# Optimization experiments

Hardware: AMD Instinct MI355X
Metric: run time of the kernel (lower is better)

## Reference

```python
import jax, jax.numpy as jnp
import numpy as np

IN_F, OUT_F, R = 4096, 4096, 16
ALPHA = 32.0
SCALING = ALPHA / R


def setup_inputs() -> dict:
    key = jax.random.key(0)
    kx, kw, ka = jax.random.split(key, 3)
    x = jax.random.normal(kx, (4, 2048, IN_F), dtype=jnp.float32)
    # xavier_normal for weight: std = sqrt(2/(fan_in+fan_out))
    std = float(np.sqrt(2.0 / (IN_F + OUT_F)))
    weight = jax.random.normal(kw, (OUT_F, IN_F), dtype=jnp.float32) * std
    bias = jnp.zeros((OUT_F,), dtype=jnp.float32)
    A = jax.random.normal(ka, (R, IN_F), dtype=jnp.float32) * 0.01
    # B initialized to zeros in the module, but use small random values so the
    # LoRA path is numerically exercised for kernel correctness testing.
    B = jax.random.normal(jax.random.fold_in(key, 7), (OUT_F, R), dtype=jnp.float32) * 0.01
    return {"x": x, "weight": weight, "bias": bias, "A": A, "B": B}


def reference(x, weight, bias, A, B):
    # out = x @ W^T + bias + scaling * ((x @ A^T) @ B^T)
    out = jnp.einsum('bsi,oi->bso', x, weight) + bias
    xa = jnp.einsum('bsi,ri->bsr', x, A)           # [b, s, r] low-rank projection
    out = out + SCALING * jnp.einsum('bsr,or->bso', xa, B)
    return out
```

## Files before the change

### kernel.cpp

```cpp
#include <hip/hip_runtime.h>
#include <hip/hip_bf16.h>
#include <cstdint>
#include <cstddef>


#define IN_F   4096
#define OUT_F  4096
#define MROWS  8192
#define RLORA  16
#define LORA_SCALE 2.0f

#define CAST_BLOCKS 32768
#define FOLD_BLOCKS 4096

#define BM   256
#define BN   256
#define BKT  32
#define NT   (IN_F / BKT)

typedef __bf16 bf16x8 __attribute__((ext_vector_type(8)));
typedef float  f32x4  __attribute__((ext_vector_type(4)));
typedef int    i32x4  __attribute__((ext_vector_type(4)));

__device__ __forceinline__ unsigned short f2bf_rne(float f) {
    union { float f; unsigned u; } v; v.f = f;
    unsigned u = v.u;
    return (unsigned short)((u + 0x7FFFu + ((u >> 16) & 1u)) >> 16);
}

__device__ __forceinline__ void gl_lds16(const unsigned short* g, unsigned short* l) {
    __builtin_amdgcn_global_load_lds(
        (const __attribute__((address_space(1))) unsigned int*)g,
        (__attribute__((address_space(3))) unsigned int*)l,
        16, 0, 0);
}


__global__ void prep_kernel(const float* __restrict__ x,
                            const float* __restrict__ W,
                            const float* __restrict__ A,
                            const float* __restrict__ B,
                            unsigned short* __restrict__ xb,
                            unsigned short* __restrict__ wb) {
    __shared__ float sB[RLORA];
    const int bid = blockIdx.x;
    if (bid < CAST_BLOCKS) {
        int i = bid * blockDim.x + threadIdx.x;
        float4 v = ((const float4*)x)[i];
        ushort4 o;
        o.x = f2bf_rne(v.x); o.y = f2bf_rne(v.y);
        o.z = f2bf_rne(v.z); o.w = f2bf_rne(v.w);
        ((ushort4*)xb)[i] = o;
    } else {
        const int o = bid - CAST_BLOCKS;
        if (threadIdx.x < RLORA) sB[threadIdx.x] = B[o * RLORA + threadIdx.x];
        __syncthreads();
        const float4* W4  = (const float4*)(W + (size_t)o * IN_F);
        ushort4*      Wp4 = (ushort4*)(wb + (size_t)o * IN_F);
        for (int i4 = threadIdx.x; i4 < IN_F / 4; i4 += blockDim.x) {
            float4 w = W4[i4];
            float ax = 0.f, ay = 0.f, az = 0.f, aw = 0.f;
            #pragma unroll
            for (int r = 0; r < RLORA; ++r) {
                float4 a = ((const float4*)(A + (size_t)r * IN_F))[i4];
                float s = sB[r];
                ax += s * a.x; ay += s * a.y; az += s * a.z; aw += s * a.w;
            }
            w.x += LORA_SCALE * ax; w.y += LORA_SCALE * ay;
            w.z += LORA_SCALE * az; w.w += LORA_SCALE * aw;
            ushort4 ov;
            ov.x = f2bf_rne(w.x); ov.y = f2bf_rne(w.y);
            ov.z = f2bf_rne(w.z); ov.w = f2bf_rne(w.w);
            Wp4[i4] = ov;
        }
    }
}


__global__ __launch_bounds__(512, 2)
void gemm_bt_bias(const unsigned short* __restrict__ Xb,
                  const unsigned short* __restrict__ Wb,
                  const float* __restrict__ bias,
                  float* __restrict__ out) {
    __shared__ __align__(16) unsigned short smem[4 * 16384];

    const int tid  = threadIdx.x;
    const int wave = tid >> 6;
    const int lane = tid & 63;
    const int quad = lane >> 4;
    const int r16  = lane & 15;
    const int wm   = wave >> 2;
    const int wn   = wave & 3;

    const int bid = blockIdx.x;
    const int xcd = bid & 7;
    const int t   = bid >> 3;
    const int n0  = (xcd * 2 + (t & 1)) * BN;
    const int m0  = (t >> 1) * BM;

    const int qA0 = wave * 128 + lane;
    const int qA1 = qA0 + 64;
    const int rA0 = qA0 >> 2, kA0 = (qA0 & 3) ^ ((rA0 >> 1) & 3);
    const int rA1 = qA1 >> 2, kA1 = (qA1 & 3) ^ ((rA1 >> 1) & 3);

    const unsigned short* gA0 = Xb + (size_t)(m0 + rA0) * IN_F + kA0 * 8;
    const unsigned short* gA1 = Xb + (size_t)(m0 + rA1) * IN_F + kA1 * 8;
    const unsigned short* gB0 = Wb + (size_t)(n0 + rA0) * IN_F + kA0 * 8;
    const unsigned short* gB1 = Wb + (size_t)(n0 + rA1) * IN_F + kA1 * 8;

    const unsigned dA0 = wave * 1024;
    const unsigned dA1 = dA0 + 512;
    const unsigned dB0 = 8192 + wave * 1024;
    const unsigned dB1 = dB0 + 512;

    const unsigned slot  = (unsigned)(quad ^ ((r16 >> 1) & 3));
    const unsigned aoff  = (unsigned)((wm * 128 + r16) * 64) + slot * 16;
    const unsigned boff  = 16384u + (unsigned)((wn * 64 + r16) * 64) + slot * 16;
    const unsigned sbase = (unsigned)(size_t)
        ((__attribute__((address_space(3))) unsigned short*)smem);

    f32x4 acc[8][4] = {};

    #pragma unroll
    for (int s = 0; s < 3; ++s) {
        unsigned short* Lb = smem + (s << 14);
        gl_lds16(gA0, Lb + dA0); gl_lds16(gA1, Lb + dA1);
        gl_lds16(gB0, Lb + dB0); gl_lds16(gB1, Lb + dB1);
        gA0 += BKT; gA1 += BKT; gB0 += BKT; gB1 += BKT;
    }
    asm volatile("s_waitcnt vmcnt(8)" ::: "memory");
    __builtin_amdgcn_s_barrier();

    for (int p = 0; p < NT; ++p) {
        if (p + 3 < NT) {
            unsigned short* Lb = smem + (((p + 3) & 3) << 14);
            gl_lds16(gA0, Lb + dA0); gl_lds16(gA1, Lb + dA1);
            gl_lds16(gB0, Lb + dB0); gl_lds16(gB1, Lb + dB1);
            gA0 += BKT; gA1 += BKT; gB0 += BKT; gB1 += BKT;
        }

        const unsigned bufb = sbase + ((unsigned)(p & 3) << 15);
        const unsigned ab = bufb + aoff;
        const unsigned bb = bufb + boff;

        i32x4 aR[8]; i32x4 bR[4];
        asm volatile("ds_read_b128 %0, %1"             : "=v"(bR[0]) : "v"(bb));
        asm volatile("ds_read_b128 %0, %1 offset:1024" : "=v"(bR[1]) : "v"(bb));
        asm volatile("ds_read_b128 %0, %1 offset:2048" : "=v"(bR[2]) : "v"(bb));
        asm volatile("ds_read_b128 %0, %1 offset:3072" : "=v"(bR[3]) : "v"(bb));
        asm volatile("ds_read_b128 %0, %1"             : "=v"(aR[0]) : "v"(ab));
        asm volatile("ds_read_b128 %0, %1 offset:1024" : "=v"(aR[1]) : "v"(ab));
        asm volatile("ds_read_b128 %0, %1 offset:2048" : "=v"(aR[2]) : "v"(ab));
        asm volatile("ds_read_b128 %0, %1 offset:3072" : "=v"(aR[3]) : "v"(ab));
        asm volatile("ds_read_b128 %0, %1 offset:4096" : "=v"(aR[4]) : "v"(ab));
        asm volatile("ds_read_b128 %0, %1 offset:5120" : "=v"(aR[5]) : "v"(ab));
        asm volatile("ds_read_b128 %0, %1 offset:6144" : "=v"(aR[6]) : "v"(ab));
        asm volatile("ds_read_b128 %0, %1 offset:7168" : "=v"(aR[7]) : "v"(ab));

        asm volatile("s_waitcnt lgkmcnt(4)" ::: "memory");
        __builtin_amdgcn_sched_barrier(0);
        __builtin_amdgcn_s_setprio(1);
        #pragma unroll
        for (int mi = 0; mi < 4; ++mi) {
            const bf16x8 a = __builtin_bit_cast(bf16x8, aR[mi]);
            #pragma unroll
            for (int nj = 0; nj < 4; ++nj)
                acc[mi][nj] = __builtin_amdgcn_mfma_f32_16x16x32_bf16(
                    a, __builtin_bit_cast(bf16x8, bR[nj]), acc[mi][nj], 0, 0, 0);
        }
        asm volatile("s_waitcnt lgkmcnt(0)" ::: "memory");
        __builtin_amdgcn_sched_barrier(0);
        #pragma unroll
        for (int mi = 4; mi < 8; ++mi) {
            const bf16x8 a = __builtin_bit_cast(bf16x8, aR[mi]);
            #pragma unroll
            for (int nj = 0; nj < 4; ++nj)
                acc[mi][nj] = __builtin_amdgcn_mfma_f32_16x16x32_bf16(
                    a, __builtin_bit_cast(bf16x8, bR[nj]), acc[mi][nj], 0, 0, 0);
        }
        __builtin_amdgcn_sched_barrier(0);
        __builtin_amdgcn_s_setprio(0);

        if (p + 3 < NT)       { asm volatile("s_waitcnt vmcnt(8)" ::: "memory"); }
        else if (p + 3 == NT) { asm volatile("s_waitcnt vmcnt(4)" ::: "memory"); }
        else                  { asm volatile("s_waitcnt vmcnt(0)" ::: "memory"); }
        __builtin_amdgcn_s_barrier();
    }

    float bv[4];
    #pragma unroll
    for (int nj = 0; nj < 4; ++nj)
        bv[nj] = bias[n0 + wn * 64 + nj * 16 + r16];

    #pragma unroll
    for (int mi = 0; mi < 8; ++mi) {
        #pragma unroll
        for (int i = 0; i < 4; ++i) {
            const int mg = m0 + wm * 128 + mi * 16 + quad * 4 + i;
            float* orow = out + (size_t)mg * OUT_F + (n0 + wn * 64 + r16);
            #pragma unroll
            for (int nj = 0; nj < 4; ++nj)
                orow[nj * 16] = acc[mi][nj][i] + bv[nj];
        }
    }
}


extern "C" void kernel_launch(void* const* d_in, const int* in_sizes, int n_in,
                              void* d_out, int out_size, void* d_ws, size_t ws_size,
                              hipStream_t stream) {
    const float* x    = (const float*)d_in[0];
    const float* W    = (const float*)d_in[1];
    const float* bias = (const float*)d_in[2];
    const float* A    = (const float*)d_in[3];
    const float* B    = (const float*)d_in[4];
    float* out = (float*)d_out;

    unsigned short* xb = (unsigned short*)d_ws;
    unsigned short* wb = xb + (size_t)MROWS * IN_F;

    prep_kernel<<<CAST_BLOCKS + FOLD_BLOCKS, 256, 0, stream>>>(x, W, A, B, xb, wb);
    gemm_bt_bias<<<(MROWS / BM) * (OUT_F / BN), 512, 0, stream>>>(xb, wb, bias, out);
}
```

Before: 531.1 us.

## Fuse fp32-to-bf16 activation cast into GEMM load pipeline

Drops the separate pass that cast x to bf16 into workspace. The GEMM now loads fp32 x tiles into registers, converts them with packed bf16 conversion instructions, and writes them to LDS, while W still streams via direct global-to-LDS loads. The pipeline is restructured to a register-staged, two-tiles-ahead schedule, which saves a full write and re-read of the bf16 activations. In exchange the GEMM reads twice as many bytes for A, uses extra VGPRs, and has less prefetch depth.

```diff
diff --git a/kernel.cpp b/kernel.cpp
--- a/kernel.cpp
+++ b/kernel.cpp
@@ -10,9 +10,6 @@
 #define RLORA  16
 #define LORA_SCALE 2.0f
 
-#define CAST_BLOCKS 32768
-#define FOLD_BLOCKS 4096
-
 #define BM   256
 #define BN   256
 #define BKT  32
@@ -35,50 +32,87 @@
         16, 0, 0);
 }
 
-
-__global__ void prep_kernel(const float* __restrict__ x,
-                            const float* __restrict__ W,
-                            const float* __restrict__ A,
-                            const float* __restrict__ B,
-                            unsigned short* __restrict__ xb,
-                            unsigned short* __restrict__ wb) {
+__device__ __forceinline__ int cvtpk(float lo, float hi) {
+    int r;
+    asm volatile("v_cvt_pk_bf16_f32 %0, %1, %2" : "=v"(r) : "v"(lo), "v"(hi));
+    return r;
+}
+
+
+__global__ void fold_w(const float* __restrict__ W,
+                       const float* __restrict__ A,
+                       const float* __restrict__ B,
+                       unsigned short* __restrict__ wb) {
     __shared__ float sB[RLORA];
-    const int bid = blockIdx.x;
-    if (bid < CAST_BLOCKS) {
-        int i = bid * blockDim.x + threadIdx.x;
-        float4 v = ((const float4*)x)[i];
-        ushort4 o;
-        o.x = f2bf_rne(v.x); o.y = f2bf_rne(v.y);
-        o.z = f2bf_rne(v.z); o.w = f2bf_rne(v.w);
-        ((ushort4*)xb)[i] = o;
-    } else {
-        const int o = bid - CAST_BLOCKS;
-        if (threadIdx.x < RLORA) sB[threadIdx.x] = B[o * RLORA + threadIdx.x];
-        __syncthreads();
-        const float4* W4  = (const float4*)(W + (size_t)o * IN_F);
-        ushort4*      Wp4 = (ushort4*)(wb + (size_t)o * IN_F);
-        for (int i4 = threadIdx.x; i4 < IN_F / 4; i4 += blockDim.x) {
-            float4 w = W4[i4];
-            float ax = 0.f, ay = 0.f, az = 0.f, aw = 0.f;
-            #pragma unroll
-            for (int r = 0; r < RLORA; ++r) {
-                float4 a = ((const float4*)(A + (size_t)r * IN_F))[i4];
-                float s = sB[r];
-                ax += s * a.x; ay += s * a.y; az += s * a.z; aw += s * a.w;
-            }
-            w.x += LORA_SCALE * ax; w.y += LORA_SCALE * ay;
-            w.z += LORA_SCALE * az; w.w += LORA_SCALE * aw;
-            ushort4 ov;
-            ov.x = f2bf_rne(w.x); ov.y = f2bf_rne(w.y);
-            ov.z = f2bf_rne(w.z); ov.w = f2bf_rne(w.w);
-            Wp4[i4] = ov;
+    const int o = blockIdx.x;
+    if (threadIdx.x < RLORA) sB[threadIdx.x] = B[o * RLORA + threadIdx.x];
+    __syncthreads();
+    const float4* W4  = (const float4*)(W + (size_t)o * IN_F);
+    ushort4*      Wp4 = (ushort4*)(wb + (size_t)o * IN_F);
+    for (int i4 = threadIdx.x; i4 < IN_F / 4; i4 += blockDim.x) {
+        float4 w = W4[i4];
+        float ax = 0.f, ay = 0.f, az = 0.f, aw = 0.f;
+        #pragma unroll
+        for (int r = 0; r < RLORA; ++r) {
+            float4 a = ((const float4*)(A + (size_t)r * IN_F))[i4];
+            float s = sB[r];
+            ax += s * a.x; ay += s * a.y; az += s * a.z; aw += s * a.w;
         }
-    }
-}
-
+        w.x += LORA_SCALE * ax; w.y += LORA_SCALE * ay;
+        w.z += LORA_SCALE * az; w.w += LORA_SCALE * aw;
+        ushort4 ov;
+        ov.x = f2bf_rne(w.x); ov.y = f2bf_rne(w.y);
+        ov.z = f2bf_rne(w.z); ov.w = f2bf_rne(w.w);
+        Wp4[i4] = ov;
+    }
+}
+
+
+__device__ __forceinline__ void mfma_phase(unsigned bufb, unsigned aoff, unsigned boff,
+                                           f32x4 (&acc)[8][4]) {
+    const unsigned ab = bufb + aoff;
+    const unsigned bb = bufb + boff;
+    i32x4 aR[8]; i32x4 bR[4];
+    asm volatile("ds_read_b128 %0, %1"             : "=v"(bR[0]) : "v"(bb));
+    asm volatile("ds_read_b128 %0, %1 offset:1024" : "=v"(bR[1]) : "v"(bb));
+    asm volatile("ds_read_b128 %0, %1 offset:2048" : "=v"(bR[2]) : "v"(bb));
+    asm volatile("ds_read_b128 %0, %1 offset:3072" : "=v"(bR[3]) : "v"(bb));
+    asm volatile("ds_read_b128 %0, %1"             : "=v"(aR[0]) : "v"(ab));
+    asm volatile("ds_read_b128 %0, %1 offset:1024" : "=v"(aR[1]) : "v"(ab));
+    asm volatile("ds_read_b128 %0, %1 offset:2048" : "=v"(aR[2]) : "v"(ab));
+    asm volatile("ds_read_b128 %0, %1 offset:3072" : "=v"(aR[3]) : "v"(ab));
+    asm volatile("ds_read_b128 %0, %1 offset:4096" : "=v"(aR[4]) : "v"(ab));
+    asm volatile("ds_read_b128 %0, %1 offset:5120" : "=v"(aR[5]) : "v"(ab));
+    asm volatile("ds_read_b128 %0, %1 offset:6144" : "=v"(aR[6]) : "v"(ab));
+    asm volatile("ds_read_b128 %0, %1 offset:7168" : "=v"(aR[7]) : "v"(ab));
+
+    asm volatile("s_waitcnt lgkmcnt(4)" ::: "memory");
+    __builtin_amdgcn_sched_barrier(0);
+    __builtin_amdgcn_s_setprio(1);
+    #pragma unroll
+    for (int mi = 0; mi < 4; ++mi) {
+        const bf16x8 a = __builtin_bit_cast(bf16x8, aR[mi]);
+        #pragma unroll
+        for (int nj = 0; nj < 4; ++nj)
+            acc[mi][nj] = __builtin_amdgcn_mfma_f32_16x16x32_bf16(
+                a, __builtin_bit_cast(bf16x8, bR[nj]), acc[mi][nj], 0, 0, 0);
+    }
+    asm volatile("s_waitcnt lgkmcnt(0)" ::: "memory");
+    __builtin_amdgcn_sched_barrier(0);
+    #pragma unroll
+    for (int mi = 4; mi < 8; ++mi) {
+        const bf16x8 a = __builtin_bit_cast(bf16x8, aR[mi]);
+        #pragma unroll
+        for (int nj = 0; nj < 4; ++nj)
+            acc[mi][nj] = __builtin_amdgcn_mfma_f32_16x16x32_bf16(
+                a, __builtin_bit_cast(bf16x8, bR[nj]), acc[mi][nj], 0, 0, 0);
+    }
+    __builtin_amdgcn_sched_barrier(0);
+    __builtin_amdgcn_s_setprio(0);
+}
 
 __global__ __launch_bounds__(512, 2)
-void gemm_bt_bias(const unsigned short* __restrict__ Xb,
+void gemm_bt_bias(const float* __restrict__ X,
                   const unsigned short* __restrict__ Wb,
                   const float* __restrict__ bias,
                   float* __restrict__ out) {
@@ -98,20 +132,20 @@
     const int n0  = (xcd * 2 + (t & 1)) * BN;
     const int m0  = (t >> 1) * BM;
 
-    const int qA0 = wave * 128 + lane;
-    const int qA1 = qA0 + 64;
-    const int rA0 = qA0 >> 2, kA0 = (qA0 & 3) ^ ((rA0 >> 1) & 3);
-    const int rA1 = qA1 >> 2, kA1 = (qA1 & 3) ^ ((rA1 >> 1) & 3);
-
-    const unsigned short* gA0 = Xb + (size_t)(m0 + rA0) * IN_F + kA0 * 8;
-    const unsigned short* gA1 = Xb + (size_t)(m0 + rA1) * IN_F + kA1 * 8;
-    const unsigned short* gB0 = Wb + (size_t)(n0 + rA0) * IN_F + kA0 * 8;
-    const unsigned short* gB1 = Wb + (size_t)(n0 + rA1) * IN_F + kA1 * 8;
-
-    const unsigned dA0 = wave * 1024;
-    const unsigned dA1 = dA0 + 512;
+    const int q0  = wave * 128 + lane;
+    const int q1  = q0 + 64;
+    const int r0  = q0 >> 2, k0c = (q0 & 3) ^ ((r0 >> 1) & 3);
+    const int r1  = q1 >> 2, k1c = (q1 & 3) ^ ((r1 >> 1) & 3);
+
+    const float*          gA0 = X  + (size_t)(m0 + r0) * IN_F + k0c * 8;
+    const float*          gA1 = X  + (size_t)(m0 + r1) * IN_F + k1c * 8;
+    const unsigned short* gB0 = Wb + (size_t)(n0 + r0) * IN_F + k0c * 8;
+    const unsigned short* gB1 = Wb + (size_t)(n0 + r1) * IN_F + k1c * 8;
+
     const unsigned dB0 = 8192 + wave * 1024;
     const unsigned dB1 = dB0 + 512;
+    const unsigned wA0 = (unsigned)(wave * 1024 + lane * 8);
+    const unsigned wA1 = wA0 + 512;
 
     const unsigned slot  = (unsigned)(quad ^ ((r16 >> 1) & 3));
     const unsigned aoff  = (unsigned)((wm * 128 + r16) * 64) + slot * 16;
@@ -120,72 +154,58 @@
         ((__attribute__((address_space(3))) unsigned short*)smem);
 
     f32x4 acc[8][4] = {};
-
-    #pragma unroll
-    for (int s = 0; s < 3; ++s) {
-        unsigned short* Lb = smem + (s << 14);
-        gl_lds16(gA0, Lb + dA0); gl_lds16(gA1, Lb + dA1);
-        gl_lds16(gB0, Lb + dB0); gl_lds16(gB1, Lb + dB1);
-        gA0 += BKT; gA1 += BKT; gB0 += BKT; gB1 += BKT;
-    }
-    asm volatile("s_waitcnt vmcnt(8)" ::: "memory");
+    f32x4 s0, s1, s2, s3;
+
+#define STAGE_ISSUE(TILE) {                                              \
+    unsigned short* Lb = smem + (((TILE) & 3) << 14);                    \
+    s0 = ((const f32x4*)gA0)[0]; s1 = ((const f32x4*)gA0)[1];            \
+    s2 = ((const f32x4*)gA1)[0]; s3 = ((const f32x4*)gA1)[1];            \
+    gA0 += BKT; gA1 += BKT;                                              \
+    gl_lds16(gB0, Lb + dB0); gl_lds16(gB1, Lb + dB1);                    \
+    gB0 += BKT; gB1 += BKT; }
+
+#define CVT_WR(TILE) {                                                   \
+    unsigned short* Bp = smem + (((TILE) & 3) << 14);                    \
+    i32x4 w0, w1;                                                        \
+    w0[0] = cvtpk(s0[0], s0[1]);  w0[1] = cvtpk(s0[2], s0[3]);           \
+    w0[2] = cvtpk(s1[0], s1[1]);  w0[3] = cvtpk(s1[2], s1[3]);           \
+    w1[0] = cvtpk(s2[0], s2[1]);  w1[1] = cvtpk(s2[2], s2[3]);           \
+    w1[2] = cvtpk(s3[0], s3[1]);  w1[3] = cvtpk(s3[2], s3[3]);           \
+    *(i32x4*)(Bp + wA0) = w0;                                            \
+    *(i32x4*)(Bp + wA1) = w1; }
+
+    STAGE_ISSUE(0)
+    asm volatile("s_waitcnt vmcnt(2)" ::: "memory");
+    __builtin_amdgcn_sched_barrier(0);
+    CVT_WR(0)
+    STAGE_ISSUE(1)
+    asm volatile("s_waitcnt vmcnt(6)" ::: "memory");
+    asm volatile("s_waitcnt lgkmcnt(0)" ::: "memory");
     __builtin_amdgcn_s_barrier();
 
-    for (int p = 0; p < NT; ++p) {
-        if (p + 3 < NT) {
-            unsigned short* Lb = smem + (((p + 3) & 3) << 14);
-            gl_lds16(gA0, Lb + dA0); gl_lds16(gA1, Lb + dA1);
-            gl_lds16(gB0, Lb + dB0); gl_lds16(gB1, Lb + dB1);
-            gA0 += BKT; gA1 += BKT; gB0 += BKT; gB1 += BKT;
-        }
-
-        const unsigned bufb = sbase + ((unsigned)(p & 3) << 15);
-        const unsigned ab = bufb + aoff;
-        const unsigned bb = bufb + boff;
-
-        i32x4 aR[8]; i32x4 bR[4];
-        asm volatile("ds_read_b128 %0, %1"             : "=v"(bR[0]) : "v"(bb));
-        asm volatile("ds_read_b128 %0, %1 offset:1024" : "=v"(bR[1]) : "v"(bb));
-        asm volatile("ds_read_b128 %0, %1 offset:2048" : "=v"(bR[2]) : "v"(bb));
-        asm volatile("ds_read_b128 %0, %1 offset:3072" : "=v"(bR[3]) : "v"(bb));
-        asm volatile("ds_read_b128 %0, %1"             : "=v"(aR[0]) : "v"(ab));
-        asm volatile("ds_read_b128 %0, %1 offset:1024" : "=v"(aR[1]) : "v"(ab));
-        asm volatile("ds_read_b128 %0, %1 offset:2048" : "=v"(aR[2]) : "v"(ab));
-        asm volatile("ds_read_b128 %0, %1 offset:3072" : "=v"(aR[3]) : "v"(ab));
-        asm volatile("ds_read_b128 %0, %1 offset:4096" : "=v"(aR[4]) : "v"(ab));
-        asm volatile("ds_read_b128 %0, %1 offset:5120" : "=v"(aR[5]) : "v"(ab));
-        asm volatile("ds_read_b128 %0, %1 offset:6144" : "=v"(aR[6]) : "v"(ab));
-        asm volatile("ds_read_b128 %0, %1 offset:7168" : "=v"(aR[7]) : "v"(ab));
-
-        asm volatile("s_waitcnt lgkmcnt(4)" ::: "memory");
+    for (int p = 0; p < NT - 2; ++p) {
+        asm volatile("s_waitcnt vmcnt(2)" ::: "memory");
         __builtin_amdgcn_sched_barrier(0);
-        __builtin_amdgcn_s_setprio(1);
-        #pragma unroll
-        for (int mi = 0; mi < 4; ++mi) {
-            const bf16x8 a = __builtin_bit_cast(bf16x8, aR[mi]);
-            #pragma unroll
-            for (int nj = 0; nj < 4; ++nj)
-                acc[mi][nj] = __builtin_amdgcn_mfma_f32_16x16x32_bf16(
-                    a, __builtin_bit_cast(bf16x8, bR[nj]), acc[mi][nj], 0, 0, 0);
-        }
+        CVT_WR(p + 1)
+        STAGE_ISSUE(p + 2)
+        __builtin_amdgcn_sched_barrier(0);
+        mfma_phase(sbase + ((unsigned)(p & 3) << 15), aoff, boff, acc);
+        asm volatile("s_waitcnt vmcnt(6)" ::: "memory");
         asm volatile("s_waitcnt lgkmcnt(0)" ::: "memory");
-        __builtin_amdgcn_sched_barrier(0);
-        #pragma unroll
-        for (int mi = 4; mi < 8; ++mi) {
-            const bf16x8 a = __builtin_bit_cast(bf16x8, aR[mi]);
-            #pragma unroll
-            for (int nj = 0; nj < 4; ++nj)
-                acc[mi][nj] = __builtin_amdgcn_mfma_f32_16x16x32_bf16(
-                    a, __builtin_bit_cast(bf16x8, bR[nj]), acc[mi][nj], 0, 0, 0);
-        }
-        __builtin_amdgcn_sched_barrier(0);
-        __builtin_amdgcn_s_setprio(0);
-
-        if (p + 3 < NT)       { asm volatile("s_waitcnt vmcnt(8)" ::: "memory"); }
-        else if (p + 3 == NT) { asm volatile("s_waitcnt vmcnt(4)" ::: "memory"); }
-        else                  { asm volatile("s_waitcnt vmcnt(0)" ::: "memory"); }
         __builtin_amdgcn_s_barrier();
     }
+    asm volatile("s_waitcnt vmcnt(2)" ::: "memory");
+    __builtin_amdgcn_sched_barrier(0);
+    CVT_WR(NT - 1)
+    __builtin_amdgcn_sched_barrier(0);
+    mfma_phase(sbase + ((unsigned)((NT - 2) & 3) << 15), aoff, boff, acc);
+    asm volatile("s_waitcnt vmcnt(0)" ::: "memory");
+    asm volatile("s_waitcnt lgkmcnt(0)" ::: "memory");
+    __builtin_amdgcn_s_barrier();
+    mfma_phase(sbase + ((unsigned)((NT - 1) & 3) << 15), aoff, boff, acc);
+
+#undef STAGE_ISSUE
+#undef CVT_WR
 
     float bv[4];
     #pragma unroll
@@ -216,9 +236,8 @@
     const float* B    = (const float*)d_in[4];
     float* out = (float*)d_out;
 
-    unsigned short* xb = (unsigned short*)d_ws;
-    unsigned short* wb = xb + (size_t)MROWS * IN_F;
-
-    prep_kernel<<<CAST_BLOCKS + FOLD_BLOCKS, 256, 0, stream>>>(x, W, A, B, xb, wb);
-    gemm_bt_bias<<<(MROWS / BM) * (OUT_F / BN), 512, 0, stream>>>(xb, wb, bias, out);
-}
+    unsigned short* wb = (unsigned short*)d_ws;
+
+    fold_w<<<OUT_F, 256, 0, stream>>>(W, A, B, wb);
+    gemm_bt_bias<<<(MROWS / BM) * (OUT_F / BN), 512, 0, stream>>>(x, wb, bias, out);
+}
```

Result: slower. 556.7 us (+4.8%).

## Tile LoRA weight fold, widen cast per thread, interleave LDS reads with MFMAs

Applied to the files above, without the earlier changes.

The prep kernel's weight-fold path now stages a 16x256 slice of A and a 128-row slice of B in shared memory, so each block folds 128 output rows over 256 columns and reuses A from registers. Before, every output row reread all of A from global memory. The x cast now converts 8 floats per thread, which halves the number of cast blocks. In the GEMM, the per-tile LDS reads are split into chunks that are issued between groups of MFMAs, so LDS latency overlaps with matrix math instead of the math waiting on most of the reads up front. The finer-grained waitcnt sequencing adds scheduling complexity and the risk of stalls if the lgkmcnt counts are off.

```diff
diff --git a/kernel.cpp b/kernel.cpp
--- a/kernel.cpp
+++ b/kernel.cpp
@@ -10,8 +10,8 @@
 #define RLORA  16
 #define LORA_SCALE 2.0f
 
-#define CAST_BLOCKS 32768
-#define FOLD_BLOCKS 4096
+#define CAST_BLOCKS 16384
+#define FOLD_BLOCKS 512
 
 #define BM   256
 #define BN   256
@@ -42,40 +42,135 @@
                             const float* __restrict__ B,
                             unsigned short* __restrict__ xb,
                             unsigned short* __restrict__ wb) {
-    __shared__ float sB[RLORA];
+    __shared__ float4 sA4[16 * 64];
+    __shared__ float4 sB4[128 * 4];
     const int bid = blockIdx.x;
+    const int tid = threadIdx.x;
+
     if (bid < CAST_BLOCKS) {
-        int i = bid * blockDim.x + threadIdx.x;
-        float4 v = ((const float4*)x)[i];
-        ushort4 o;
-        o.x = f2bf_rne(v.x); o.y = f2bf_rne(v.y);
-        o.z = f2bf_rne(v.z); o.w = f2bf_rne(v.w);
-        ((ushort4*)xb)[i] = o;
-    } else {
-        const int o = bid - CAST_BLOCKS;
-        if (threadIdx.x < RLORA) sB[threadIdx.x] = B[o * RLORA + threadIdx.x];
-        __syncthreads();
-        const float4* W4  = (const float4*)(W + (size_t)o * IN_F);
-        ushort4*      Wp4 = (ushort4*)(wb + (size_t)o * IN_F);
-        for (int i4 = threadIdx.x; i4 < IN_F / 4; i4 += blockDim.x) {
-            float4 w = W4[i4];
-            float ax = 0.f, ay = 0.f, az = 0.f, aw = 0.f;
-            #pragma unroll
-            for (int r = 0; r < RLORA; ++r) {
-                float4 a = ((const float4*)(A + (size_t)r * IN_F))[i4];
-                float s = sB[r];
-                ax += s * a.x; ay += s * a.y; az += s * a.z; aw += s * a.w;
-            }
-            w.x += LORA_SCALE * ax; w.y += LORA_SCALE * ay;
-            w.z += LORA_SCALE * az; w.w += LORA_SCALE * aw;
-            ushort4 ov;
-            ov.x = f2bf_rne(w.x); ov.y = f2bf_rne(w.y);
-            ov.z = f2bf_rne(w.z); ov.w = f2bf_rne(w.w);
-            Wp4[i4] = ov;
+        const int i = bid * 256 + tid;
+        float4 v0 = ((const float4*)x)[i * 2];
+        float4 v1 = ((const float4*)x)[i * 2 + 1];
+        ushort4 o0, o1;
+        o0.x = f2bf_rne(v0.x); o0.y = f2bf_rne(v0.y);
+        o0.z = f2bf_rne(v0.z); o0.w = f2bf_rne(v0.w);
+        o1.x = f2bf_rne(v1.x); o1.y = f2bf_rne(v1.y);
+        o1.z = f2bf_rne(v1.z); o1.w = f2bf_rne(v1.w);
+        ((ushort4*)xb)[i * 2]     = o0;
+        ((ushort4*)xb)[i * 2 + 1] = o1;
+        return;
+    }
+
+    const int fb = bid - CAST_BLOCKS;
+    const int ic = fb & 15;
+    const int oc = fb >> 4;
+    const int c0 = ic * 256;
+    const int o0 = oc * 128;
+
+    for (int t = tid; t < 1024; t += 256) {
+        const int r = t >> 6, c = t & 63;
+        sA4[t] = ((const float4*)(A + (size_t)r * IN_F + c0))[c];
+    }
+    for (int t = tid; t < 512; t += 256)
+        sB4[t] = ((const float4*)(B + (size_t)o0 * RLORA))[t];
+    __syncthreads();
+
+    const int c4 = tid & 63;
+    const int og = tid >> 6;
+    float4 a[RLORA];
+    #pragma unroll
+    for (int r = 0; r < RLORA; ++r) a[r] = sA4[r * 64 + c4];
+
+    for (int i = 0; i < 32; ++i) {
+        const int ol = og * 32 + i;
+        const int o  = o0 + ol;
+        float4 w = ((const float4*)(W + (size_t)o * IN_F + c0))[c4];
+        const float4 q0 = sB4[ol * 4 + 0];
+        const float4 q1 = sB4[ol * 4 + 1];
+        const float4 q2 = sB4[ol * 4 + 2];
+        const float4 q3 = sB4[ol * 4 + 3];
+        const float s[RLORA] = {q0.x,q0.y,q0.z,q0.w, q1.x,q1.y,q1.z,q1.w,
+                                q2.x,q2.y,q2.z,q2.w, q3.x,q3.y,q3.z,q3.w};
+        float ax = 0.f, ay = 0.f, az = 0.f, aw = 0.f;
+        #pragma unroll
+        for (int r = 0; r < RLORA; ++r) {
+            ax += s[r] * a[r].x; ay += s[r] * a[r].y;
+            az += s[r] * a[r].z; aw += s[r] * a[r].w;
         }
-    }
-}
-
+        w.x += LORA_SCALE * ax; w.y += LORA_SCALE * ay;
+        w.z += LORA_SCALE * az; w.w += LORA_SCALE * aw;
+        ushort4 ov;
+        ov.x = f2bf_rne(w.x); ov.y = f2bf_rne(w.y);
+        ov.z = f2bf_rne(w.z); ov.w = f2bf_rne(w.w);
+        ((ushort4*)(wb + (size_t)o * IN_F + c0))[c4] = ov;
+    }
+}
+
+
+__device__ __forceinline__ void mfma_phase(unsigned bufb, unsigned aoff, unsigned boff,
+                                           f32x4 (&acc)[8][4]) {
+    const unsigned ab = bufb + aoff;
+    const unsigned bb = bufb + boff;
+    i32x4 aR[8]; i32x4 bR[4];
+    asm volatile("ds_read_b128 %0, %1"             : "=v"(bR[0]) : "v"(bb));
+    asm volatile("ds_read_b128 %0, %1 offset:1024" : "=v"(bR[1]) : "v"(bb));
+    asm volatile("ds_read_b128 %0, %1 offset:2048" : "=v"(bR[2]) : "v"(bb));
+    asm volatile("ds_read_b128 %0, %1 offset:3072" : "=v"(bR[3]) : "v"(bb));
+    asm volatile("ds_read_b128 %0, %1"             : "=v"(aR[0]) : "v"(ab));
+    asm volatile("ds_read_b128 %0, %1 offset:1024" : "=v"(aR[1]) : "v"(ab));
+    asm volatile("ds_read_b128 %0, %1 offset:2048" : "=v"(aR[2]) : "v"(ab));
+    asm volatile("ds_read_b128 %0, %1 offset:3072" : "=v"(aR[3]) : "v"(ab));
+
+    asm volatile("s_waitcnt lgkmcnt(2)" ::: "memory");
+    __builtin_amdgcn_sched_barrier(0);
+    asm volatile("ds_read_b128 %0, %1 offset:4096" : "=v"(aR[4]) : "v"(ab));
+    asm volatile("ds_read_b128 %0, %1 offset:5120" : "=v"(aR[5]) : "v"(ab));
+    __builtin_amdgcn_sched_barrier(0);
+    __builtin_amdgcn_s_setprio(1);
+    #pragma unroll
+    for (int mi = 0; mi < 2; ++mi) {
+        const bf16x8 a = __builtin_bit_cast(bf16x8, aR[mi]);
+        #pragma unroll
+        for (int nj = 0; nj < 4; ++nj)
+            acc[mi][nj] = __builtin_amdgcn_mfma_f32_16x16x32_bf16(
+                a, __builtin_bit_cast(bf16x8, bR[nj]), acc[mi][nj], 0, 0, 0);
+    }
+    asm volatile("s_waitcnt lgkmcnt(2)" ::: "memory");
+    __builtin_amdgcn_sched_barrier(0);
+    asm volatile("ds_read_b128 %0, %1 offset:6144" : "=v"(aR[6]) : "v"(ab));
+    asm volatile("ds_read_b128 %0, %1 offset:7168" : "=v"(aR[7]) : "v"(ab));
+    __builtin_amdgcn_sched_barrier(0);
+    #pragma unroll
+    for (int mi = 2; mi < 4; ++mi) {
+        const bf16x8 a = __builtin_bit_cast(bf16x8, aR[mi]);
+        #pragma unroll
+        for (int nj = 0; nj < 4; ++nj)
+            acc[mi][nj] = __builtin_amdgcn_mfma_f32_16x16x32_bf16(
+                a, __builtin_bit_cast(bf16x8, bR[nj]), acc[mi][nj], 0, 0, 0);
+    }
+    asm volatile("s_waitcnt lgkmcnt(2)" ::: "memory");
+    __builtin_amdgcn_sched_barrier(0);
+    #pragma unroll
+    for (int mi = 4; mi < 6; ++mi) {
+        const bf16x8 a = __builtin_bit_cast(bf16x8, aR[mi]);
+        #pragma unroll
+        for (int nj = 0; nj < 4; ++nj)
+            acc[mi][nj] = __builtin_amdgcn_mfma_f32_16x16x32_bf16(
+                a, __builtin_bit_cast(bf16x8, bR[nj]), acc[mi][nj], 0, 0, 0);
+    }
+    asm volatile("s_waitcnt lgkmcnt(0)" ::: "memory");
+    __builtin_amdgcn_sched_barrier(0);
+    #pragma unroll
+    for (int mi = 6; mi < 8; ++mi) {
+        const bf16x8 a = __builtin_bit_cast(bf16x8, aR[mi]);
+        #pragma unroll
+        for (int nj = 0; nj < 4; ++nj)
+            acc[mi][nj] = __builtin_amdgcn_mfma_f32_16x16x32_bf16(
+                a, __builtin_bit_cast(bf16x8, bR[nj]), acc[mi][nj], 0, 0, 0);
+    }
+    __builtin_amdgcn_sched_barrier(0);
+    __builtin_amdgcn_s_setprio(0);
+}
 
 __global__ __launch_bounds__(512, 2)
 void gemm_bt_bias(const unsigned short* __restrict__ Xb,
@@ -98,20 +193,20 @@
     const int n0  = (xcd * 2 + (t & 1)) * BN;
     const int m0  = (t >> 1) * BM;
 
-    const int qA0 = wave * 128 + lane;
-    const int qA1 = qA0 + 64;
-    const int rA0 = qA0 >> 2, kA0 = (qA0 & 3) ^ ((rA0 >> 1) & 3);
-    const int rA1 = qA1 >> 2, kA1 = (qA1 & 3) ^ ((rA1 >> 1) & 3);
-
-    const unsigned short* gA0 = Xb + (size_t)(m0 + rA0) * IN_F + kA0 * 8;
-    const unsigned short* gA1 = Xb + (size_t)(m0 + rA1) * IN_F + kA1 * 8;
-    const unsigned short* gB0 = Wb + (size_t)(n0 + rA0) * IN_F + kA0 * 8;
-    const unsigned short* gB1 = Wb + (size_t)(n0 + rA1) * IN_F + kA1 * 8;
-
-    const unsigned dA0 = wave * 1024;
-    const unsigned dA1 = dA0 + 512;
-    const unsigned dB0 = 8192 + wave * 1024;
-    const unsigned dB1 = dB0 + 512;
+    const int q0  = wave * 128 + lane;
+    const int q1  = q0 + 64;
+    const int r0  = q0 >> 2, k0c = (q0 & 3) ^ ((r0 >> 1) & 3);
+    const int r1  = q1 >> 2, k1c = (q1 & 3) ^ ((r1 >> 1) & 3);
+
+    const unsigned short* gA0 = Xb + (size_t)(m0 + r0) * IN_F + k0c * 8;
+    const unsigned short* gA1 = Xb + (size_t)(m0 + r1) * IN_F + k1c * 8;
+    const unsigned short* gB0 = Wb + (size_t)(n0 + r0) * IN_F + k0c * 8;
+    const unsigned short* gB1 = Wb + (size_t)(n0 + r1) * IN_F + k1c * 8;
+
+    unsigned short* const lA0 = smem + wave * 1024;
+    unsigned short* const lA1 = lA0 + 512;
+    unsigned short* const lB0 = smem + 8192 + wave * 1024;
+    unsigned short* const lB1 = lB0 + 512;
 
     const unsigned slot  = (unsigned)(quad ^ ((r16 >> 1) & 3));
     const unsigned aoff  = (unsigned)((wm * 128 + r16) * 64) + slot * 16;
@@ -121,71 +216,25 @@
 
     f32x4 acc[8][4] = {};
 
-    #pragma unroll
-    for (int s = 0; s < 3; ++s) {
-        unsigned short* Lb = smem + (s << 14);
-        gl_lds16(gA0, Lb + dA0); gl_lds16(gA1, Lb + dA1);
-        gl_lds16(gB0, Lb + dB0); gl_lds16(gB1, Lb + dB1);
-        gA0 += BKT; gA1 += BKT; gB0 += BKT; gB1 += BKT;
-    }
+#define STAGE(TILE) {                                                    \
+    const unsigned off = (unsigned)(((TILE) & 3) << 14);                 \
+    gl_lds16(gA0, lA0 + off); gl_lds16(gA1, lA1 + off);                  \
+    gl_lds16(gB0, lB0 + off); gl_lds16(gB1, lB1 + off);                  \
+    gA0 += BKT; gA1 += BKT; gB0 += BKT; gB1 += BKT; }
+
+    STAGE(0) STAGE(1) STAGE(2)
     asm volatile("s_waitcnt vmcnt(8)" ::: "memory");
     __builtin_amdgcn_s_barrier();
 
     for (int p = 0; p < NT; ++p) {
-        if (p + 3 < NT) {
-            unsigned short* Lb = smem + (((p + 3) & 3) << 14);
-            gl_lds16(gA0, Lb + dA0); gl_lds16(gA1, Lb + dA1);
-            gl_lds16(gB0, Lb + dB0); gl_lds16(gB1, Lb + dB1);
-            gA0 += BKT; gA1 += BKT; gB0 += BKT; gB1 += BKT;
-        }
-
-        const unsigned bufb = sbase + ((unsigned)(p & 3) << 15);
-        const unsigned ab = bufb + aoff;
-        const unsigned bb = bufb + boff;
-
-        i32x4 aR[8]; i32x4 bR[4];
-        asm volatile("ds_read_b128 %0, %1"             : "=v"(bR[0]) : "v"(bb));
-        asm volatile("ds_read_b128 %0, %1 offset:1024" : "=v"(bR[1]) : "v"(bb));
-        asm volatile("ds_read_b128 %0, %1 offset:2048" : "=v"(bR[2]) : "v"(bb));
-        asm volatile("ds_read_b128 %0, %1 offset:3072" : "=v"(bR[3]) : "v"(bb));
-        asm volatile("ds_read_b128 %0, %1"             : "=v"(aR[0]) : "v"(ab));
-        asm volatile("ds_read_b128 %0, %1 offset:1024" : "=v"(aR[1]) : "v"(ab));
-        asm volatile("ds_read_b128 %0, %1 offset:2048" : "=v"(aR[2]) : "v"(ab));
-        asm volatile("ds_read_b128 %0, %1 offset:3072" : "=v"(aR[3]) : "v"(ab));
-        asm volatile("ds_read_b128 %0, %1 offset:4096" : "=v"(aR[4]) : "v"(ab));
-        asm volatile("ds_read_b128 %0, %1 offset:5120" : "=v"(aR[5]) : "v"(ab));
-        asm volatile("ds_read_b128 %0, %1 offset:6144" : "=v"(aR[6]) : "v"(ab));
-        asm volatile("ds_read_b128 %0, %1 offset:7168" : "=v"(aR[7]) : "v"(ab));
-
-        asm volatile("s_waitcnt lgkmcnt(4)" ::: "memory");
-        __builtin_amdgcn_sched_barrier(0);
-        __builtin_amdgcn_s_setprio(1);
-        #pragma unroll
-        for (int mi = 0; mi < 4; ++mi) {
-            const bf16x8 a = __builtin_bit_cast(bf16x8, aR[mi]);
-            #pragma unroll
-            for (int nj = 0; nj < 4; ++nj)
-                acc[mi][nj] = __builtin_amdgcn_mfma_f32_16x16x32_bf16(
-                    a, __builtin_bit_cast(bf16x8, bR[nj]), acc[mi][nj], 0, 0, 0);
-        }
-        asm volatile("s_waitcnt lgkmcnt(0)" ::: "memory");
-        __builtin_amdgcn_sched_barrier(0);
-        #pragma unroll
-        for (int mi = 4; mi < 8; ++mi) {
-            const bf16x8 a = __builtin_bit_cast(bf16x8, aR[mi]);
-            #pragma unroll
-            for (int nj = 0; nj < 4; ++nj)
-                acc[mi][nj] = __builtin_amdgcn_mfma_f32_16x16x32_bf16(
-                    a, __builtin_bit_cast(bf16x8, bR[nj]), acc[mi][nj], 0, 0, 0);
-        }
-        __builtin_amdgcn_sched_barrier(0);
-        __builtin_amdgcn_s_setprio(0);
-
+        if (p + 3 < NT) STAGE(p + 3)
+        mfma_phase(sbase + ((unsigned)(p & 3) << 15), aoff, boff, acc);
         if (p + 3 < NT)       { asm volatile("s_waitcnt vmcnt(8)" ::: "memory"); }
         else if (p + 3 == NT) { asm volatile("s_waitcnt vmcnt(4)" ::: "memory"); }
         else                  { asm volatile("s_waitcnt vmcnt(0)" ::: "memory"); }
         __builtin_amdgcn_s_barrier();
     }
+#undef STAGE
 
     float bv[4];
     #pragma unroll
```

Result: slower. 631.6 us (+18.9%).

## Split GEMM main loop into two phases interleaving A/B global loads with MFMA

Applied to the files above, without the earlier changes.

Restructures the K-loop into two half-phases: each phase issues a subset of LDS reads plus half of the global-to-LDS prefetch (A tile then B tile), separated by extra workgroup barriers, then runs half the MFMAs. The goal is to spread memory issue across the compute and synchronise waves so loads and MFMA interleave, in the style of a ping-pong schedule. It adds three extra barriers per iteration and halves the A fragment register footprint, at the risk of more synchronisation stalls.

```diff
diff --git a/kernel.cpp b/kernel.cpp
--- a/kernel.cpp
+++ b/kernel.cpp
@@ -98,20 +98,20 @@
     const int n0  = (xcd * 2 + (t & 1)) * BN;
     const int m0  = (t >> 1) * BM;
 
-    const int qA0 = wave * 128 + lane;
-    const int qA1 = qA0 + 64;
-    const int rA0 = qA0 >> 2, kA0 = (qA0 & 3) ^ ((rA0 >> 1) & 3);
-    const int rA1 = qA1 >> 2, kA1 = (qA1 & 3) ^ ((rA1 >> 1) & 3);
-
-    const unsigned short* gA0 = Xb + (size_t)(m0 + rA0) * IN_F + kA0 * 8;
-    const unsigned short* gA1 = Xb + (size_t)(m0 + rA1) * IN_F + kA1 * 8;
-    const unsigned short* gB0 = Wb + (size_t)(n0 + rA0) * IN_F + kA0 * 8;
-    const unsigned short* gB1 = Wb + (size_t)(n0 + rA1) * IN_F + kA1 * 8;
-
-    const unsigned dA0 = wave * 1024;
-    const unsigned dA1 = dA0 + 512;
-    const unsigned dB0 = 8192 + wave * 1024;
-    const unsigned dB1 = dB0 + 512;
+    const int q0  = wave * 128 + lane;
+    const int q1  = q0 + 64;
+    const int r0  = q0 >> 2, k0c = (q0 & 3) ^ ((r0 >> 1) & 3);
+    const int r1  = q1 >> 2, k1c = (q1 & 3) ^ ((r1 >> 1) & 3);
+
+    const unsigned short* gA0 = Xb + (size_t)(m0 + r0) * IN_F + k0c * 8;
+    const unsigned short* gA1 = Xb + (size_t)(m0 + r1) * IN_F + k1c * 8;
+    const unsigned short* gB0 = Wb + (size_t)(n0 + r0) * IN_F + k0c * 8;
+    const unsigned short* gB1 = Wb + (size_t)(n0 + r1) * IN_F + k1c * 8;
+
+    unsigned short* const lA0 = smem + wave * 1024;
+    unsigned short* const lA1 = lA0 + 512;
+    unsigned short* const lB0 = smem + 8192 + wave * 1024;
+    unsigned short* const lB1 = lB0 + 512;
 
     const unsigned slot  = (unsigned)(quad ^ ((r16 >> 1) & 3));
     const unsigned aoff  = (unsigned)((wm * 128 + r16) * 64) + slot * 16;
@@ -121,29 +121,27 @@
 
     f32x4 acc[8][4] = {};
 
-    #pragma unroll
-    for (int s = 0; s < 3; ++s) {
-        unsigned short* Lb = smem + (s << 14);
-        gl_lds16(gA0, Lb + dA0); gl_lds16(gA1, Lb + dA1);
-        gl_lds16(gB0, Lb + dB0); gl_lds16(gB1, Lb + dB1);
-        gA0 += BKT; gA1 += BKT; gB0 += BKT; gB1 += BKT;
-    }
+#define STAGE_A(TILE) {                                                  \
+    const unsigned off = (unsigned)(((TILE) & 3) << 14);                 \
+    gl_lds16(gA0, lA0 + off); gl_lds16(gA1, lA1 + off);                  \
+    gA0 += BKT; gA1 += BKT; }
+#define STAGE_B(TILE) {                                                  \
+    const unsigned off = (unsigned)(((TILE) & 3) << 14);                 \
+    gl_lds16(gB0, lB0 + off); gl_lds16(gB1, lB1 + off);                  \
+    gB0 += BKT; gB1 += BKT; }
+
+    STAGE_A(0) STAGE_B(0)
+    STAGE_A(1) STAGE_B(1)
+    STAGE_A(2) STAGE_B(2)
     asm volatile("s_waitcnt vmcnt(8)" ::: "memory");
     __builtin_amdgcn_s_barrier();
 
     for (int p = 0; p < NT; ++p) {
-        if (p + 3 < NT) {
-            unsigned short* Lb = smem + (((p + 3) & 3) << 14);
-            gl_lds16(gA0, Lb + dA0); gl_lds16(gA1, Lb + dA1);
-            gl_lds16(gB0, Lb + dB0); gl_lds16(gB1, Lb + dB1);
-            gA0 += BKT; gA1 += BKT; gB0 += BKT; gB1 += BKT;
-        }
-
         const unsigned bufb = sbase + ((unsigned)(p & 3) << 15);
         const unsigned ab = bufb + aoff;
         const unsigned bb = bufb + boff;
 
-        i32x4 aR[8]; i32x4 bR[4];
+        i32x4 aR[4], bR[4], aS[4];
         asm volatile("ds_read_b128 %0, %1"             : "=v"(bR[0]) : "v"(bb));
         asm volatile("ds_read_b128 %0, %1 offset:1024" : "=v"(bR[1]) : "v"(bb));
         asm volatile("ds_read_b128 %0, %1 offset:2048" : "=v"(bR[2]) : "v"(bb));
@@ -152,12 +150,9 @@
         asm volatile("ds_read_b128 %0, %1 offset:1024" : "=v"(aR[1]) : "v"(ab));
         asm volatile("ds_read_b128 %0, %1 offset:2048" : "=v"(aR[2]) : "v"(ab));
         asm volatile("ds_read_b128 %0, %1 offset:3072" : "=v"(aR[3]) : "v"(ab));
-        asm volatile("ds_read_b128 %0, %1 offset:4096" : "=v"(aR[4]) : "v"(ab));
-        asm volatile("ds_read_b128 %0, %1 offset:5120" : "=v"(aR[5]) : "v"(ab));
-        asm volatile("ds_read_b128 %0, %1 offset:6144" : "=v"(aR[6]) : "v"(ab));
-        asm volatile("ds_read_b128 %0, %1 offset:7168" : "=v"(aR[7]) : "v"(ab));
-
-        asm volatile("s_waitcnt lgkmcnt(4)" ::: "memory");
+        if (p + 3 < NT) STAGE_A(p + 3)
+        __builtin_amdgcn_s_barrier();
+        asm volatile("s_waitcnt lgkmcnt(0)" ::: "memory");
         __builtin_amdgcn_sched_barrier(0);
         __builtin_amdgcn_s_setprio(1);
         #pragma unroll
@@ -168,24 +163,36 @@
                 acc[mi][nj] = __builtin_amdgcn_mfma_f32_16x16x32_bf16(
                     a, __builtin_bit_cast(bf16x8, bR[nj]), acc[mi][nj], 0, 0, 0);
         }
+        __builtin_amdgcn_sched_barrier(0);
+        __builtin_amdgcn_s_setprio(0);
+        __builtin_amdgcn_s_barrier();
+
+        asm volatile("ds_read_b128 %0, %1 offset:4096" : "=v"(aS[0]) : "v"(ab));
+        asm volatile("ds_read_b128 %0, %1 offset:5120" : "=v"(aS[1]) : "v"(ab));
+        asm volatile("ds_read_b128 %0, %1 offset:6144" : "=v"(aS[2]) : "v"(ab));
+        asm volatile("ds_read_b128 %0, %1 offset:7168" : "=v"(aS[3]) : "v"(ab));
+        if (p + 3 < NT) STAGE_B(p + 3)
+        __builtin_amdgcn_s_barrier();
         asm volatile("s_waitcnt lgkmcnt(0)" ::: "memory");
         __builtin_amdgcn_sched_barrier(0);
+        __builtin_amdgcn_s_setprio(1);
         #pragma unroll
-        for (int mi = 4; mi < 8; ++mi) {
-            const bf16x8 a = __builtin_bit_cast(bf16x8, aR[mi]);
+        for (int mi = 0; mi < 4; ++mi) {
+            const bf16x8 a = __builtin_bit_cast(bf16x8, aS[mi]);
             #pragma unroll
             for (int nj = 0; nj < 4; ++nj)
-                acc[mi][nj] = __builtin_amdgcn_mfma_f32_16x16x32_bf16(
-                    a, __builtin_bit_cast(bf16x8, bR[nj]), acc[mi][nj], 0, 0, 0);
+                acc[mi + 4][nj] = __builtin_amdgcn_mfma_f32_16x16x32_bf16(
+                    a, __builtin_bit_cast(bf16x8, bR[nj]), acc[mi + 4][nj], 0, 0, 0);
         }
         __builtin_amdgcn_sched_barrier(0);
         __builtin_amdgcn_s_setprio(0);
-
         if (p + 3 < NT)       { asm volatile("s_waitcnt vmcnt(8)" ::: "memory"); }
         else if (p + 3 == NT) { asm volatile("s_waitcnt vmcnt(4)" ::: "memory"); }
         else                  { asm volatile("s_waitcnt vmcnt(0)" ::: "memory"); }
         __builtin_amdgcn_s_barrier();
     }
+#undef STAGE_A
+#undef STAGE_B
 
     float bv[4];
     #pragma unroll
```

Measured after the change: 549.1 us. 3.4% more time.
